# Kernel optimization log

Measured on AMD Instinct MI355X. Metric: run time of the kernel, lower is better.

Reference implementation:

```python
import jax, jax.numpy as jnp
import numpy as np

EPS = 1e-12  # torch F.normalize eps

def setup_inputs() -> dict:
    key = jax.random.key(0)
    k1, k2 = jax.random.split(key)
    N, M, D = 256, 2000, 128
    gene_seq = jax.random.randint(k1, (N, M), 0, 4)
    embedding_mat = jax.random.normal(k2, (M, 4, D), dtype=jnp.float32) * (np.sqrt(2.0) / D)
    return {"gene_seq": gene_seq, "embedding_mat": embedding_mat}

def reference(gene_seq, embedding_mat):
    # L2-normalize each (gene, base) row along embedding dim (torch F.normalize semantics)
    norm = jnp.linalg.norm(embedding_mat, axis=-1, keepdims=True)
    table = embedding_mat / jnp.maximum(norm, EPS)  # (M, 4, D)
    M = table.shape[0]
    # One-hot einsum 'nmi,nmid->nmd' == direct gather of row gene_seq[n,m] at position m
    gene_idx = jnp.arange(M)[None, :]               # (1, M)
    out = table[gene_idx, gene_seq, :]              # (N, M, D)
    return out
```

## Files before the change

kernel.cpp:

```cpp
#include <hip/hip_runtime.h>


#define N_SEQ   256
#define M_GENES 2000
#define D_DIM   128
#define J_PER_N (M_GENES * D_DIM / 4)

__global__ __launch_bounds__(256) void GeneEmbedder_kernel(
    const int*   __restrict__ gene_seq,
    const float* __restrict__ emb,
    float*       __restrict__ out)
{
    const int n = blockIdx.y;
    const int j = blockIdx.x * 256 + threadIdx.x;
    const int m = j >> 5;
    const int c = j & 31;

    const int g = gene_seq[n * M_GENES + m];

    const float4 v = *reinterpret_cast<const float4*>(
        emb + ((((m << 2) + g) << 7) + (c << 2)));

    float ss = v.x * v.x + v.y * v.y + v.z * v.z + v.w * v.w;
    ss += __shfl_xor(ss, 1, 32);
    ss += __shfl_xor(ss, 2, 32);
    ss += __shfl_xor(ss, 4, 32);
    ss += __shfl_xor(ss, 8, 32);
    ss += __shfl_xor(ss, 16, 32);

    const float inv = 1.0f / fmaxf(sqrtf(ss), 1e-12f);

    float4 o;
    o.x = v.x * inv;
    o.y = v.y * inv;
    o.z = v.z * inv;
    o.w = v.w * inv;

    *reinterpret_cast<float4*>(
        out + (size_t)n * (M_GENES * D_DIM) + ((size_t)j << 2)) = o;
}

extern "C" void kernel_launch(void* const* d_in, const int* in_sizes, int n_in,
                              void* d_out, int out_size, void* d_ws, size_t ws_size,
                              hipStream_t stream) {
    const int*   gene_seq = (const int*)d_in[0];
    const float* emb      = (const float*)d_in[1];
    float*       out      = (float*)d_out;

    dim3 grid(J_PER_N / 256, N_SEQ, 1);
    dim3 block(256, 1, 1);
    GeneEmbedder_kernel<<<grid, block, 0, stream>>>(gene_seq, emb, out);
}
```

Measured before the change: 295.2 us.

## Precompute per-row inverse norms, then gather-scale with nontemporal stores

Splits the work into two kernels. The first computes one inverse L2 norm per (gene, base) row into workspace. The second gathers rows, scales them by the precomputed value, and writes output with nontemporal stores, processing 10 float4 per thread. This removes the per-output shuffle reduction, which is recomputed 256 times per row, and aims to reduce cache pollution from the large output stream. The cost is an extra launch and a small workspace read.

```diff
diff --git a/kernel.cpp b/kernel.cpp
--- a/kernel.cpp
+++ b/kernel.cpp
@@ -4,40 +4,57 @@
 #define N_SEQ   256
 #define M_GENES 2000
 #define D_DIM   128
-#define J_PER_N (M_GENES * D_DIM / 4)
+#define ROWS    (M_GENES * 4)
+#define P2_BX   25
+#define P2_IT   10
 
-__global__ __launch_bounds__(256) void GeneEmbedder_kernel(
-    const int*   __restrict__ gene_seq,
+typedef float vfloat4 __attribute__((ext_vector_type(4)));
+
+__global__ __launch_bounds__(256) void inv_norm_kernel(
     const float* __restrict__ emb,
-    float*       __restrict__ out)
+    float*       __restrict__ inv_norm)
 {
-    const int n = blockIdx.y;
-    const int j = blockIdx.x * 256 + threadIdx.x;
-    const int m = j >> 5;
-    const int c = j & 31;
+    const int idx = blockIdx.x * 256 + threadIdx.x;
+    const int row = idx >> 5;
+    const int c   = idx & 31;
 
-    const int g = gene_seq[n * M_GENES + m];
-
-    const float4 v = *reinterpret_cast<const float4*>(
-        emb + ((((m << 2) + g) << 7) + (c << 2)));
-
+    const vfloat4 v = *reinterpret_cast<const vfloat4*>(emb + ((row << 7) + (c << 2)));
     float ss = v.x * v.x + v.y * v.y + v.z * v.z + v.w * v.w;
     ss += __shfl_xor(ss, 1, 32);
     ss += __shfl_xor(ss, 2, 32);
     ss += __shfl_xor(ss, 4, 32);
     ss += __shfl_xor(ss, 8, 32);
     ss += __shfl_xor(ss, 16, 32);
+    const float inv = 1.0f / fmaxf(sqrtf(ss), 1e-12f);
+    if (c == 0) inv_norm[row] = inv;
+}
 
-    const float inv = 1.0f / fmaxf(sqrtf(ss), 1e-12f);
+__global__ __launch_bounds__(256) void gather_scale_kernel(
+    const int*   __restrict__ gene_seq,
+    const float* __restrict__ emb,
+    const float* __restrict__ inv_norm,
+    float*       __restrict__ out)
+{
+    const int n = blockIdx.y;
+    const int* __restrict__ gs = gene_seq + n * M_GENES;
+    float* __restrict__ outn = out + (size_t)n * (M_GENES * D_DIM);
 
-    float4 o;
-    o.x = v.x * inv;
-    o.y = v.y * inv;
-    o.z = v.z * inv;
-    o.w = v.w * inv;
+    const int j0 = blockIdx.x * 256 + threadIdx.x;
 
-    *reinterpret_cast<float4*>(
-        out + (size_t)n * (M_GENES * D_DIM) + ((size_t)j << 2)) = o;
+    #pragma unroll
+    for (int it = 0; it < P2_IT; ++it) {
+        const int j = j0 + it * (P2_BX * 256);
+        const int m = j >> 5;
+        const int c = j & 31;
+
+        const int   g   = gs[m];
+        const int   row = (m << 2) + g;
+        const float inv = inv_norm[row];
+        const vfloat4 v = *reinterpret_cast<const vfloat4*>(emb + ((row << 7) + (c << 2)));
+
+        vfloat4 o = v * inv;
+        __builtin_nontemporal_store(o, reinterpret_cast<vfloat4*>(outn + ((size_t)j << 2)));
+    }
 }
 
 extern "C" void kernel_launch(void* const* d_in, const int* in_sizes, int n_in,
@@ -46,8 +63,10 @@
     const int*   gene_seq = (const int*)d_in[0];
     const float* emb      = (const float*)d_in[1];
     float*       out      = (float*)d_out;
+    float*       inv_norm = (float*)d_ws;
 
-    dim3 grid(J_PER_N / 256, N_SEQ, 1);
-    dim3 block(256, 1, 1);
-    GeneEmbedder_kernel<<<grid, block, 0, stream>>>(gene_seq, emb, out);
+    inv_norm_kernel<<<dim3(ROWS * 32 / 256), dim3(256), 0, stream>>>(emb, inv_norm);
+
+    gather_scale_kernel<<<dim3(P2_BX, N_SEQ), dim3(256), 0, stream>>>(
+        gene_seq, emb, inv_norm, out);
 }
```

After: 270.8 us. 8.2% less time.
